# Kernel optimization log

Measured on AMD Instinct MI355X. Metric: run time of the kernel, lower is better.

Reference implementation:

```python
import jax, jax.numpy as jnp
import numpy as np

N_NODES = 100000
N_EDGES = 3200000
N_GRAPHS = 64
IN_DIM = 4
HID = 64
EPS = 1e-5  # BatchNorm eps


def _batchnorm(x, gamma, beta):
    # training-mode batch norm over the node/graph axis (biased variance)
    mu = x.mean(axis=0)
    var = x.var(axis=0)
    return (x - mu) * jax.lax.rsqrt(var + EPS) * gamma + beta


def _gcn_conv(x, W, b, src, dst, n):
    # PyG GCNConv with add_self_loops=True, edge_weight=1:
    # out = D^{-1/2}(A+I)D^{-1/2} x W + b
    h = x @ W  # [N, out]
    deg = jax.ops.segment_sum(jnp.ones((src.shape[0],), h.dtype), dst,
                              num_segments=n) + 1.0  # +1 for self-loop
    dinv = jax.lax.rsqrt(deg)
    norm = dinv[src] * dinv[dst]  # [E]
    agg = jax.ops.segment_sum(h[src] * norm[:, None], dst, num_segments=n)
    # self-loop contribution: norm = 1/deg[i]
    return agg + h * (1.0 / deg)[:, None] + b


def setup_inputs() -> dict:
    key = jax.random.key(0)
    ks = jax.random.split(key, 12)
    s = 0.1
    inp = {
        "x": jax.random.normal(ks[0], (N_NODES, IN_DIM), jnp.float32),
        "edge_index": jax.random.randint(ks[1], (2, N_EDGES), 0, N_NODES, dtype=jnp.int64),
        "batch": jnp.sort(jax.random.randint(ks[2], (N_NODES,), 0, N_GRAPHS, dtype=jnp.int64)),
        # BatchNorm(4)
        "bn0_g": jnp.ones((IN_DIM,), jnp.float32),
        "bn0_b": jnp.zeros((IN_DIM,), jnp.float32),
        # GCNConv(4, 64)
        "W0": jax.random.normal(ks[3], (IN_DIM, HID), jnp.float32) * s,
        "b0": jnp.zeros((HID,), jnp.float32),
        # GCNConv(64, 64)
        "W1": jax.random.normal(ks[4], (HID, HID), jnp.float32) * s,
        "b1": jnp.zeros((HID,), jnp.float32),
        # BatchNorm(64) after pooling
        "bn1_g": jnp.ones((HID,), jnp.float32),
        "bn1_b": jnp.zeros((HID,), jnp.float32),
        # two hidden Linear(64, 64)
        "lin0_W": jax.random.normal(ks[5], (HID, HID), jnp.float32) * s,
        "lin0_b": jnp.zeros((HID,), jnp.float32),
        "lin1_W": jax.random.normal(ks[6], (HID, HID), jnp.float32) * s,
        "lin1_b": jnp.zeros((HID,), jnp.float32),
        # Linear(64, 1)
        "out_W": jax.random.normal(ks[7], (HID, 1), jnp.float32) * s,
        "out_b": jnp.zeros((1,), jnp.float32),
    }
    return inp


def reference(x, edge_index, batch, bn0_g, bn0_b, W0, b0, W1, b1,
              bn1_g, bn1_b, lin0_W, lin0_b, lin1_W, lin1_b, out_W, out_b):
    src, dst = edge_index[0], edge_index[1]
    h = _batchnorm(x, bn0_g, bn0_b)
    h = _gcn_conv(h, W0, b0, src, dst, N_NODES)
    h = _gcn_conv(h, W1, b1, src, dst, N_NODES)
    g = jax.ops.segment_sum(h, batch, num_segments=N_GRAPHS)  # global_add_pool
    g = _batchnorm(g, bn1_g, bn1_b)
    g = g @ lin0_W + lin0_b
    g = g @ lin1_W + lin1_b
    return g @ out_W + out_b  # [N_GRAPHS, 1]
```

## Files before the change

kernel.cpp:

```cpp
#include <hip/hip_runtime.h>
#include <hip/hip_bf16.h>

#define EPSF 1e-5f

static constexpr int NGRAPH = 64;
static constexpr int HBA = 512;
static constexpr int SH = 9;
static constexpr int GB = 256;
static constexpr int CAP = 128;
static constexpr int CAPN = 88;
static constexpr int NBLK = 512;
static constexpr int BNB = 64;
static constexpr int NEL = NGRAPH * 6 + NGRAPH * 4;
static constexpr int RCH = 4;

__global__ __launch_bounds__(256) void k_scat(const float4* __restrict__ x,
                                              int N, const int* __restrict__ ei,
                                              int E, int chunk,
                                              float* __restrict__ bnpart,
                                              unsigned* __restrict__ counts,
                                              unsigned* __restrict__ bedges) {
  __shared__ unsigned cur[256];
  __shared__ float red[4][8];
  int t = threadIdx.x;
  if (blockIdx.x < GB) {
    int g = blockIdx.x;
    cur[t] = 0;
    __syncthreads();
    int lo = g * chunk, hi = min(E, lo + chunk);
    size_t segbase = (size_t)g * 256 * CAP;
    for (int base = lo + 8 * t; base < hi; base += 8 * 256) {
      int nv = min(8, hi - base);
      int s[8], d[8];
#pragma unroll
      for (int j = 0; j < 8; j++) {
        s[j] = (j < nv) ? ei[base + j] : 0;
        d[j] = (j < nv) ? ei[E + base + j] : 0;
      }
      unsigned pos[8], bb[8];
#pragma unroll
      for (int j = 0; j < 8; j++)
        if (j < nv) {
          bb[j] = (unsigned)d[j] >> SH;
          pos[j] = atomicAdd(&cur[bb[j]], 1u);
        }
#pragma unroll
      for (int j = 0; j < 8; j++)
        if (j < nv && pos[j] < (unsigned)CAP)
          bedges[segbase + (size_t)bb[j] * CAP + pos[j]] =
              ((unsigned)s[j] << SH) | (unsigned)(d[j] & (HBA - 1));
    }
    __syncthreads();
    counts[(size_t)g * 256 + t] = min(cur[t], (unsigned)CAP);
  } else {
    int g2 = blockIdx.x - GB;
    float s[4] = {0, 0, 0, 0}, q[4] = {0, 0, 0, 0};
    for (int i = g2 * 256 + t; i < N; i += BNB * 256) {
      float4 v = x[i];
      s[0] += v.x; q[0] += v.x * v.x;
      s[1] += v.y; q[1] += v.y * v.y;
      s[2] += v.z; q[2] += v.z * v.z;
      s[3] += v.w; q[3] += v.w * v.w;
    }
#pragma unroll
    for (int o = 32; o > 0; o >>= 1) {
#pragma unroll
      for (int k = 0; k < 4; k++) {
        s[k] += __shfl_down(s[k], o);
        q[k] += __shfl_down(q[k], o);
      }
    }
    int w = t >> 6;
    if ((t & 63) == 0) {
#pragma unroll
      for (int k = 0; k < 4; k++) {
        red[w][k] = s[k];
        red[w][4 + k] = q[k];
      }
    }
    __syncthreads();
    if (t < 8) {
      float a = red[0][t] + red[1][t] + red[2][t] + red[3][t];
      bnpart[g2 * 8 + t] = a;
    }
  }
}

__device__ __forceinline__ void bn0_coefs(const float* __restrict__ stats,
                                          const float* __restrict__ g,
                                          const float* __restrict__ b,
                                          float Ninv, float* sc, float* sh) {
#pragma unroll
  for (int k = 0; k < 4; k++) {
    float mu = stats[k] * Ninv;
    float var = stats[4 + k] * Ninv - mu * mu;
    var = var < 0.f ? 0.f : var;
    float s = g[k] / sqrtf(var + EPSF);
    sc[k] = s;
    sh[k] = b[k] - mu * s;
  }
}

__global__ __launch_bounds__(512) void k_build(
    const unsigned* __restrict__ bedges, const unsigned* __restrict__ counts,
    const float4* __restrict__ x, int N, const float* __restrict__ bnpart,
    const float* __restrict__ bn0g, const float* __restrict__ bn0b,
    float Ninv, uint4* __restrict__ pk, unsigned* __restrict__ csr) {
  __shared__ unsigned cur[HBA];
  __shared__ unsigned scnt[256];
  __shared__ float sstats[8];
  int t = threadIdx.x;
  int r = blockIdx.x;
  cur[t] = 0;
  if (t < 256) scnt[t] = counts[(size_t)t * 256 + r];
  else if (t < 264) {
    int e = t - 256;
    float s = 0.f;
#pragma unroll 8
    for (int i = 0; i < BNB; i++) s += bnpart[i * 8 + e];
    sstats[e] = s;
  }
  __syncthreads();
  int wv = t >> 6, ln = t & 63;
  size_t nodeBase = (size_t)((unsigned)r << SH) * CAPN;
  for (int g = wv; g < 256; g += 8) {
    unsigned cnt = scnt[g];
    const unsigned* seg = bedges + ((size_t)g * 256 + r) * CAP;
    for (unsigned i = ln; i < cnt; i += 64) {
      unsigned p = seg[i];
      unsigned rel = p & (HBA - 1);
      unsigned pos = atomicAdd(&cur[rel], 1u);
      if (pos < (unsigned)CAPN)
        csr[nodeBase + (size_t)rel * CAPN + pos] = p >> SH;
    }
  }
  __syncthreads();
  unsigned deg = min(cur[t], (unsigned)CAPN);
  int v = (r << SH) + t;
  if (v < N) {
    float sco[4], sho[4];
    bn0_coefs(sstats, bn0g, bn0b, Ninv, sco, sho);
    float dv = rsqrtf((float)deg + 1.0f);
    float4 xv = x[v];
    float zx = dv * (xv.x * sco[0] + sho[0]);
    float zy = dv * (xv.y * sco[1] + sho[1]);
    float zz = dv * (xv.z * sco[2] + sho[2]);
    float zw = dv * (xv.w * sco[3] + sho[3]);
    uint4 u;
    u.x = (__float_as_uint(zx) & ~15u) | (deg & 15u);
    u.y = (__float_as_uint(zy) & ~15u) | ((deg >> 4) & 15u);
    u.z = (__float_as_uint(zz) & ~15u) | ((deg >> 8) & 15u);
    u.w = (__float_as_uint(zw) & ~15u) | ((deg >> 12) & 15u);
    pk[v] = u;
  }
}

__global__ __launch_bounds__(256) void k_acc1f(
    const unsigned* __restrict__ csr, const uint4* __restrict__ pk,
    const int* __restrict__ batch, int N, uint4* __restrict__ p2,
    float* __restrict__ part1) {
  __shared__ float lac[NGRAPH * 6];
  for (int i = threadIdx.x; i < NGRAPH * 6; i += blockDim.x) lac[i] = 0.f;
  __syncthreads();
  int total = gridDim.x * blockDim.x;
  int iters = (N + total - 1) / total;
  int v = blockIdx.x * blockDim.x + threadIdx.x;
  for (int it = 0; it < iters; ++it, v += total) {
    bool act = v < N;
    float u0 = 0, u1 = 0, u2 = 0, u3 = 0, sv = 0, cv = 0;
    int g = 0;
    if (act) {
      uint4 qv = pk[v];
      unsigned deg = (qv.x & 15u) | ((qv.y & 15u) << 4) |
                     ((qv.z & 15u) << 8) | ((qv.w & 15u) << 12);
      unsigned degP = (deg + 3u) & ~3u;
      const uint4* cp = (const uint4*)(csr + (size_t)v * CAPN);
      float a0 = 0, a1 = 0, a2 = 0, a3 = 0, asd = 0;
      for (unsigned e = 0; e < degP; e += 8) {
        uint4 i0 = cp[e >> 2];
        uint4 i1 = cp[(e >> 2) + 1];
        unsigned s[8] = {i0.x, i0.y, i0.z, i0.w, i1.x, i1.y, i1.z, i1.w};
        int m = (int)(deg - e);
        uint4 q[8];
#pragma unroll
        for (int j = 0; j < 8; j++)
          if (j < m) q[j] = pk[s[j]];
#pragma unroll
        for (int j = 0; j < 8; j++)
          if (j < m) {
            unsigned dg = (q[j].x & 15u) | ((q[j].y & 15u) << 4) |
                          ((q[j].z & 15u) << 8) | ((q[j].w & 15u) << 12);
            asd += rsqrtf((float)dg + 1.0f);
            a0 += __uint_as_float(q[j].x);
            a1 += __uint_as_float(q[j].y);
            a2 += __uint_as_float(q[j].z);
            a3 += __uint_as_float(q[j].w);
          }
      }
      float dv = rsqrtf((float)deg + 1.0f);
      float idg = dv * dv;
      float px = idg * (a0 + __uint_as_float(qv.x));
      float py = idg * (a1 + __uint_as_float(qv.y));
      float pz = idg * (a2 + __uint_as_float(qv.z));
      float pw = idg * (a3 + __uint_as_float(qv.w));
      uint4 o;
      o.x = (__float_as_uint(px) & ~15u) | (deg & 15u);
      o.y = (__float_as_uint(py) & ~15u) | ((deg >> 4) & 15u);
      o.z = (__float_as_uint(pz) & ~15u) | ((deg >> 8) & 15u);
      o.w = (__float_as_uint(pw) & ~15u) | ((deg >> 12) & 15u);
      p2[v] = o;
      g = batch[v];
      u0 = dv * __uint_as_float(o.x);
      u1 = dv * __uint_as_float(o.y);
      u2 = dv * __uint_as_float(o.z);
      u3 = dv * __uint_as_float(o.w);
      sv = idg + dv * asd;
      cv = 1.0f;
    }
    if (__all(!act)) continue;
    int gf = __shfl(g, 0);
    bool uni = __all((!act) || (g == gf));
    if (uni) {
#pragma unroll
      for (int o = 32; o > 0; o >>= 1) {
        u0 += __shfl_down(u0, o);
        u1 += __shfl_down(u1, o);
        u2 += __shfl_down(u2, o);
        u3 += __shfl_down(u3, o);
        sv += __shfl_down(sv, o);
        cv += __shfl_down(cv, o);
      }
      if ((threadIdx.x & 63) == 0) {
        int g6 = gf * 6;
        atomicAdd(&lac[g6 + 0], u0);
        atomicAdd(&lac[g6 + 1], u1);
        atomicAdd(&lac[g6 + 2], u2);
        atomicAdd(&lac[g6 + 3], u3);
        atomicAdd(&lac[g6 + 4], sv);
        atomicAdd(&lac[g6 + 5], cv);
      }
    } else if (act) {
      int g6 = g * 6;
      atomicAdd(&lac[g6 + 0], u0);
      atomicAdd(&lac[g6 + 1], u1);
      atomicAdd(&lac[g6 + 2], u2);
      atomicAdd(&lac[g6 + 3], u3);
      atomicAdd(&lac[g6 + 4], sv);
      atomicAdd(&lac[g6 + 5], cv);
    }
  }
  __syncthreads();
  float* out = part1 + (size_t)blockIdx.x * (NGRAPH * 6);
  for (int i = threadIdx.x; i < NGRAPH * 6; i += blockDim.x) out[i] = lac[i];
}

__global__ __launch_bounds__(256) void k_acc2f(
    const unsigned* __restrict__ csr, const uint4* __restrict__ p2,
    const int* __restrict__ batch, int N, float* __restrict__ part2) {
  __shared__ float lac[NGRAPH * 4];
  for (int i = threadIdx.x; i < NGRAPH * 4; i += blockDim.x) lac[i] = 0.f;
  __syncthreads();
  int total = gridDim.x * blockDim.x;
  int iters = (N + total - 1) / total;
  int v = blockIdx.x * blockDim.x + threadIdx.x;
  for (int it = 0; it < iters; ++it, v += total) {
    bool act = v < N;
    float u0 = 0, u1 = 0, u2 = 0, u3 = 0;
    int g = 0;
    if (act) {
      uint4 pv = p2[v];
      unsigned deg = (pv.x & 15u) | ((pv.y & 15u) << 4) |
                     ((pv.z & 15u) << 8) | ((pv.w & 15u) << 12);
      unsigned degP = (deg + 3u) & ~3u;
      const uint4* cp = (const uint4*)(csr + (size_t)v * CAPN);
      float t0 = 0, t1 = 0, t2 = 0, t3 = 0;
      for (unsigned e = 0; e < degP; e += 8) {
        uint4 i0 = cp[e >> 2];
        uint4 i1 = cp[(e >> 2) + 1];
        unsigned s[8] = {i0.x, i0.y, i0.z, i0.w, i1.x, i1.y, i1.z, i1.w};
        int m = (int)(deg - e);
        uint4 q[8];
#pragma unroll
        for (int j = 0; j < 8; j++)
          if (j < m) q[j] = p2[s[j]];
#pragma unroll
        for (int j = 0; j < 8; j++)
          if (j < m) {
            t0 += __uint_as_float(q[j].x);
            t1 += __uint_as_float(q[j].y);
            t2 += __uint_as_float(q[j].z);
            t3 += __uint_as_float(q[j].w);
          }
      }
      float dv = rsqrtf((float)deg + 1.0f);
      g = batch[v];
      u0 = dv * t0; u1 = dv * t1; u2 = dv * t2; u3 = dv * t3;
    }
    if (__all(!act)) continue;
    int gf = __shfl(g, 0);
    bool uni = __all((!act) || (g == gf));
    if (uni) {
#pragma unroll
      for (int o = 32; o > 0; o >>= 1) {
        u0 += __shfl_down(u0, o);
        u1 += __shfl_down(u1, o);
        u2 += __shfl_down(u2, o);
        u3 += __shfl_down(u3, o);
      }
      if ((threadIdx.x & 63) == 0) {
        int g4 = gf * 4;
        atomicAdd(&lac[g4 + 0], u0);
        atomicAdd(&lac[g4 + 1], u1);
        atomicAdd(&lac[g4 + 2], u2);
        atomicAdd(&lac[g4 + 3], u3);
      }
    } else if (act) {
      int g4 = g * 4;
      atomicAdd(&lac[g4 + 0], u0);
      atomicAdd(&lac[g4 + 1], u1);
      atomicAdd(&lac[g4 + 2], u2);
      atomicAdd(&lac[g4 + 3], u3);
    }
  }
  __syncthreads();
  float* out = part2 + (size_t)blockIdx.x * (NGRAPH * 4);
  for (int i = threadIdx.x; i < NGRAPH * 4; i += blockDim.x) out[i] = lac[i];
}

__global__ __launch_bounds__(64) void k_red(const float* __restrict__ part1,
                                            const float* __restrict__ part2,
                                            float* __restrict__ redp) {
  int bid = blockIdx.x;
  int c = bid / 10;
  int eg = bid % 10;
  int e = eg * 64 + threadIdx.x;
  if (e >= NEL) return;
  const float* src;
  int stride, idx;
  if (e < NGRAPH * 6) {
    src = part1; stride = NGRAPH * 6; idx = e;
  } else {
    src = part2; stride = NGRAPH * 4; idx = e - NGRAPH * 6;
  }
  float s = 0.f;
  int b0 = c * (NBLK / RCH);
#pragma unroll 8
  for (int b = 0; b < NBLK / RCH; b++)
    s += src[(size_t)(b0 + b) * stride + idx];
  redp[c * NEL + e] = s;
}

__global__ __launch_bounds__(1024) void k_final(
    const float* __restrict__ redp,
    const float* __restrict__ W0, const float* __restrict__ b0,
    const float* __restrict__ W1, const float* __restrict__ b1,
    const float* __restrict__ bn1g, const float* __restrict__ bn1b,
    const float* __restrict__ l0W, const float* __restrict__ l0b,
    const float* __restrict__ l1W, const float* __restrict__ l1b,
    const float* __restrict__ oW, const float* __restrict__ ob,
    float* __restrict__ out) {
  __shared__ float sP1[NGRAPH * 6];
  __shared__ float sU2[NGRAPH * 4];
  __shared__ float sW01[4 * 64];
  __shared__ float sb01[64];
  __shared__ float sA[4096];
  __shared__ float sB[4096];
  __shared__ float sSc[64], sSh[64];
  __shared__ float wW1[4096], wl0[4096], wl1[4096];
  int t = threadIdx.x;
  for (int i = t; i < 4096; i += 1024) {
    wW1[i] = W1[i];
    wl0[i] = l0W[i];
    wl1[i] = l1W[i];
  }
  if (t < NEL) {
    float s = redp[t] + redp[NEL + t] + redp[2 * NEL + t] + redp[3 * NEL + t];
    if (t < NGRAPH * 6) sP1[t] = s;
    else sU2[t - NGRAPH * 6] = s;
  }
  __syncthreads();
  if (t < 256) {
    int k = t >> 6, f = t & 63;
    float a = 0.f;
#pragma unroll
    for (int j = 0; j < 64; j++) a += W0[k * 64 + j] * wW1[j * 64 + f];
    sW01[t] = a;
  } else if (t < 320) {
    int f = t - 256;
    float a = 0.f;
#pragma unroll
    for (int j = 0; j < 64; j++) a += b0[j] * wW1[j * 64 + f];
    sb01[f] = a;
  }
  __syncthreads();
  for (int idx = t; idx < 4096; idx += 1024) {
    int G = idx >> 6, f = idx & 63;
    float v = sP1[G * 6 + 5] * b1[f] + sP1[G * 6 + 4] * sb01[f];
    v += (sU2[G * 4 + 0] + sP1[G * 6 + 0]) * sW01[0 * 64 + f];
    v += (sU2[G * 4 + 1] + sP1[G * 6 + 1]) * sW01[1 * 64 + f];
    v += (sU2[G * 4 + 2] + sP1[G * 6 + 2]) * sW01[2 * 64 + f];
    v += (sU2[G * 4 + 3] + sP1[G * 6 + 3]) * sW01[3 * 64 + f];
    sA[idx] = v;
  }
  __syncthreads();
  if (t < 64) {
    float mu = 0.f;
#pragma unroll
    for (int G = 0; G < 64; G++) mu += sA[G * 64 + t];
    mu *= (1.0f / 64.0f);
    float var = 0.f;
#pragma unroll
    for (int G = 0; G < 64; G++) {
      float d = sA[G * 64 + t] - mu;
      var += d * d;
    }
    var *= (1.0f / 64.0f);
    float s = bn1g[t] / sqrtf(var + EPSF);
    sSc[t] = s;
    sSh[t] = bn1b[t] - mu * s;
  }
  __syncthreads();
  for (int idx = t; idx < 4096; idx += 1024) {
    int f = idx & 63;
    sA[idx] = sA[idx] * sSc[f] + sSh[f];
  }
  __syncthreads();
  {
    int G = t >> 4, f0 = (t & 15) * 4;
    float a0 = l0b[f0], a1 = l0b[f0 + 1], a2 = l0b[f0 + 2], a3 = l0b[f0 + 3];
#pragma unroll
    for (int j = 0; j < 64; j++) {
      float a = sA[G * 64 + j];
      float4 w = *(const float4*)&wl0[j * 64 + f0];
      a0 += a * w.x; a1 += a * w.y; a2 += a * w.z; a3 += a * w.w;
    }
    *(float4*)&sB[G * 64 + f0] = make_float4(a0, a1, a2, a3);
  }
  __syncthreads();
  {
    int G = t >> 4, f0 = (t & 15) * 4;
    float a0 = l1b[f0], a1 = l1b[f0 + 1], a2 = l1b[f0 + 2], a3 = l1b[f0 + 3];
#pragma unroll
    for (int j = 0; j < 64; j++) {
      float a = sB[G * 64 + j];
      float4 w = *(const float4*)&wl1[j * 64 + f0];
      a0 += a * w.x; a1 += a * w.y; a2 += a * w.z; a3 += a * w.w;
    }
    *(float4*)&sA[G * 64 + f0] = make_float4(a0, a1, a2, a3);
  }
  __syncthreads();
  if (t < 64) {
    float v = ob[0];
#pragma unroll
    for (int j = 0; j < 64; j++) v += sA[t * 64 + j] * oW[j];
    out[t] = v;
  }
}

extern "C" void kernel_launch(void* const* d_in, const int* in_sizes, int n_in,
                              void* d_out, int out_size, void* d_ws,
                              size_t ws_size, hipStream_t stream) {
  const float* x = (const float*)d_in[0];
  const int* ei = (const int*)d_in[1];
  const int* batch = (const int*)d_in[2];
  const float* bn0g = (const float*)d_in[3];
  const float* bn0b = (const float*)d_in[4];
  const float* W0 = (const float*)d_in[5];
  const float* b0 = (const float*)d_in[6];
  const float* W1 = (const float*)d_in[7];
  const float* b1 = (const float*)d_in[8];
  const float* bn1g = (const float*)d_in[9];
  const float* bn1b = (const float*)d_in[10];
  const float* l0W = (const float*)d_in[11];
  const float* l0b = (const float*)d_in[12];
  const float* l1W = (const float*)d_in[13];
  const float* l1b = (const float*)d_in[14];
  const float* oW = (const float*)d_in[15];
  const float* ob = (const float*)d_in[16];

  const int N = in_sizes[0] / 4;
  const int E = in_sizes[1] / 2;
  const int RA = (N + HBA - 1) >> SH;
  const int chunk = (E + GB - 1) / GB;

  size_t off = 0;
  auto alloc = [&](size_t nbytes) {
    size_t cur = (off + 63) & ~(size_t)63;
    off = cur + nbytes;
    return (void*)((char*)d_ws + cur);
  };
  float* bnpart = (float*)alloc((size_t)BNB * 8 * 4);
  float* part1 = (float*)alloc((size_t)NBLK * NGRAPH * 6 * 4);
  float* part2 = (float*)alloc((size_t)NBLK * NGRAPH * 4 * 4);
  float* redp = (float*)alloc((size_t)RCH * NEL * 4);
  uint4* pk = (uint4*)alloc((size_t)N * 16);
  unsigned* counts = (unsigned*)alloc((size_t)GB * 256 * 4);
  unsigned* bedges = (unsigned*)alloc((size_t)GB * 256 * CAP * 4);
  unsigned* csr =
      (unsigned*)alloc(((size_t)RA * HBA * CAPN + 16) * 4);
  uint4* p2 = (uint4*)bedges;
  (void)ws_size;

  const float Ninv = 1.0f / (float)N;
  k_scat<<<GB + BNB, 256, 0, stream>>>((const float4*)x, N, ei, E, chunk,
                                       bnpart, counts, bedges);
  k_build<<<RA, 512, 0, stream>>>(bedges, counts, (const float4*)x, N, bnpart,
                                  bn0g, bn0b, Ninv, pk, csr);
  k_acc1f<<<NBLK, 256, 0, stream>>>(csr, pk, batch, N, p2, part1);
  k_acc2f<<<NBLK, 256, 0, stream>>>(csr, p2, batch, N, part2);
  k_red<<<RCH * 10, 64, 0, stream>>>(part1, part2, redp);
  k_final<<<1, 1024, 0, stream>>>(redp, W0, b0, W1, b1, bn1g, bn1b,
                                  l0W, l0b, l1W, l1b, oW, ob, (float*)d_out);
}
```

Baseline: 224.3 us.

## Split each node's neighbor gather across four lanes and widen scatter blocks

```diff
diff --git a/kernel.cpp b/kernel.cpp
--- a/kernel.cpp
+++ b/kernel.cpp
@@ -9,27 +9,27 @@
 static constexpr int GB = 256;
 static constexpr int CAP = 128;
 static constexpr int CAPN = 88;
-static constexpr int NBLK = 512;
+static constexpr int NBLK = 1568;
 static constexpr int BNB = 64;
 static constexpr int NEL = NGRAPH * 6 + NGRAPH * 4;
-static constexpr int RCH = 4;
-
-__global__ __launch_bounds__(256) void k_scat(const float4* __restrict__ x,
+static constexpr int RCH = 8;
+
+__global__ __launch_bounds__(512) void k_scat(const float4* __restrict__ x,
                                               int N, const int* __restrict__ ei,
                                               int E, int chunk,
                                               float* __restrict__ bnpart,
                                               unsigned* __restrict__ counts,
                                               unsigned* __restrict__ bedges) {
   __shared__ unsigned cur[256];
-  __shared__ float red[4][8];
+  __shared__ float red[8][8];
   int t = threadIdx.x;
   if (blockIdx.x < GB) {
     int g = blockIdx.x;
-    cur[t] = 0;
+    if (t < 256) cur[t] = 0;
     __syncthreads();
     int lo = g * chunk, hi = min(E, lo + chunk);
     size_t segbase = (size_t)g * 256 * CAP;
-    for (int base = lo + 8 * t; base < hi; base += 8 * 256) {
+    for (int base = lo + 8 * t; base < hi; base += 8 * 512) {
       int nv = min(8, hi - base);
       int s[8], d[8];
 #pragma unroll
@@ -51,11 +51,11 @@
               ((unsigned)s[j] << SH) | (unsigned)(d[j] & (HBA - 1));
     }
     __syncthreads();
-    counts[(size_t)g * 256 + t] = min(cur[t], (unsigned)CAP);
+    if (t < 256) counts[(size_t)g * 256 + t] = min(cur[t], (unsigned)CAP);
   } else {
     int g2 = blockIdx.x - GB;
     float s[4] = {0, 0, 0, 0}, q[4] = {0, 0, 0, 0};
-    for (int i = g2 * 256 + t; i < N; i += BNB * 256) {
+    for (int i = g2 * 512 + t; i < N; i += BNB * 512) {
       float4 v = x[i];
       s[0] += v.x; q[0] += v.x * v.x;
       s[1] += v.y; q[1] += v.y * v.y;
@@ -80,7 +80,9 @@
     }
     __syncthreads();
     if (t < 8) {
-      float a = red[0][t] + red[1][t] + red[2][t] + red[3][t];
+      float a = 0.f;
+#pragma unroll
+      for (int w2 = 0; w2 < 8; w2++) a += red[w2][t];
       bnpart[g2 * 8 + t] = a;
     }
   }
@@ -162,62 +164,69 @@
   __shared__ float lac[NGRAPH * 6];
   for (int i = threadIdx.x; i < NGRAPH * 6; i += blockDim.x) lac[i] = 0.f;
   __syncthreads();
-  int total = gridDim.x * blockDim.x;
-  int iters = (N + total - 1) / total;
-  int v = blockIdx.x * blockDim.x + threadIdx.x;
-  for (int it = 0; it < iters; ++it, v += total) {
-    bool act = v < N;
-    float u0 = 0, u1 = 0, u2 = 0, u3 = 0, sv = 0, cv = 0;
-    int g = 0;
-    if (act) {
-      uint4 qv = pk[v];
-      unsigned deg = (qv.x & 15u) | ((qv.y & 15u) << 4) |
-                     ((qv.z & 15u) << 8) | ((qv.w & 15u) << 12);
-      unsigned degP = (deg + 3u) & ~3u;
-      const uint4* cp = (const uint4*)(csr + (size_t)v * CAPN);
-      float a0 = 0, a1 = 0, a2 = 0, a3 = 0, asd = 0;
-      for (unsigned e = 0; e < degP; e += 8) {
-        uint4 i0 = cp[e >> 2];
-        uint4 i1 = cp[(e >> 2) + 1];
-        unsigned s[8] = {i0.x, i0.y, i0.z, i0.w, i1.x, i1.y, i1.z, i1.w};
-        int m = (int)(deg - e);
-        uint4 q[8];
-#pragma unroll
-        for (int j = 0; j < 8; j++)
-          if (j < m) q[j] = pk[s[j]];
-#pragma unroll
-        for (int j = 0; j < 8; j++)
-          if (j < m) {
-            unsigned dg = (q[j].x & 15u) | ((q[j].y & 15u) << 4) |
-                          ((q[j].z & 15u) << 8) | ((q[j].w & 15u) << 12);
-            asd += rsqrtf((float)dg + 1.0f);
-            a0 += __uint_as_float(q[j].x);
-            a1 += __uint_as_float(q[j].y);
-            a2 += __uint_as_float(q[j].z);
-            a3 += __uint_as_float(q[j].w);
-          }
-      }
-      float dv = rsqrtf((float)deg + 1.0f);
-      float idg = dv * dv;
-      float px = idg * (a0 + __uint_as_float(qv.x));
-      float py = idg * (a1 + __uint_as_float(qv.y));
-      float pz = idg * (a2 + __uint_as_float(qv.z));
-      float pw = idg * (a3 + __uint_as_float(qv.w));
-      uint4 o;
-      o.x = (__float_as_uint(px) & ~15u) | (deg & 15u);
-      o.y = (__float_as_uint(py) & ~15u) | ((deg >> 4) & 15u);
-      o.z = (__float_as_uint(pz) & ~15u) | ((deg >> 8) & 15u);
-      o.w = (__float_as_uint(pw) & ~15u) | ((deg >> 12) & 15u);
-      p2[v] = o;
-      g = batch[v];
-      u0 = dv * __uint_as_float(o.x);
-      u1 = dv * __uint_as_float(o.y);
-      u2 = dv * __uint_as_float(o.z);
-      u3 = dv * __uint_as_float(o.w);
-      sv = idg + dv * asd;
-      cv = 1.0f;
-    }
-    if (__all(!act)) continue;
+  int tid = blockIdx.x * blockDim.x + threadIdx.x;
+  int v = tid >> 2, k = tid & 3;
+  bool act = v < N;
+  float a0 = 0, a1 = 0, a2 = 0, a3 = 0, asd = 0;
+  uint4 qv;
+  unsigned deg = 0;
+  if (act) {
+    qv = pk[v];
+    deg = (qv.x & 15u) | ((qv.y & 15u) << 4) | ((qv.z & 15u) << 8) |
+          ((qv.w & 15u) << 12);
+    const uint4* cp = (const uint4*)(csr + (size_t)v * CAPN);
+    for (unsigned e = 4 * k; e < deg; e += 16) {
+      uint4 i0 = cp[e >> 2];
+      unsigned s[4] = {i0.x, i0.y, i0.z, i0.w};
+      int m = (int)(deg - e);
+      uint4 q[4];
+#pragma unroll
+      for (int j = 0; j < 4; j++)
+        if (j < m) q[j] = pk[s[j]];
+#pragma unroll
+      for (int j = 0; j < 4; j++)
+        if (j < m) {
+          unsigned dg = (q[j].x & 15u) | ((q[j].y & 15u) << 4) |
+                        ((q[j].z & 15u) << 8) | ((q[j].w & 15u) << 12);
+          asd += rsqrtf((float)dg + 1.0f);
+          a0 += __uint_as_float(q[j].x);
+          a1 += __uint_as_float(q[j].y);
+          a2 += __uint_as_float(q[j].z);
+          a3 += __uint_as_float(q[j].w);
+        }
+    }
+  }
+#pragma unroll
+  for (int o = 1; o <= 2; o <<= 1) {
+    a0 += __shfl_xor(a0, o);
+    a1 += __shfl_xor(a1, o);
+    a2 += __shfl_xor(a2, o);
+    a3 += __shfl_xor(a3, o);
+    asd += __shfl_xor(asd, o);
+  }
+  float u0 = 0, u1 = 0, u2 = 0, u3 = 0, sv = 0, cv = 0;
+  if (act && k == 0) {
+    float dv = rsqrtf((float)deg + 1.0f);
+    float idg = dv * dv;
+    float px = idg * (a0 + __uint_as_float(qv.x));
+    float py = idg * (a1 + __uint_as_float(qv.y));
+    float pz = idg * (a2 + __uint_as_float(qv.z));
+    float pw = idg * (a3 + __uint_as_float(qv.w));
+    uint4 o;
+    o.x = (__float_as_uint(px) & ~15u) | (deg & 15u);
+    o.y = (__float_as_uint(py) & ~15u) | ((deg >> 4) & 15u);
+    o.z = (__float_as_uint(pz) & ~15u) | ((deg >> 8) & 15u);
+    o.w = (__float_as_uint(pw) & ~15u) | ((deg >> 12) & 15u);
+    p2[v] = o;
+    u0 = dv * __uint_as_float(o.x);
+    u1 = dv * __uint_as_float(o.y);
+    u2 = dv * __uint_as_float(o.z);
+    u3 = dv * __uint_as_float(o.w);
+    sv = idg + dv * asd;
+    cv = 1.0f;
+  }
+  int g = act ? batch[v] : 0;
+  if (!__all(!act)) {
     int gf = __shfl(g, 0);
     bool uni = __all((!act) || (g == gf));
     if (uni) {
@@ -239,7 +248,7 @@
         atomicAdd(&lac[g6 + 4], sv);
         atomicAdd(&lac[g6 + 5], cv);
       }
-    } else if (act) {
+    } else if (act && k == 0) {
       int g6 = g * 6;
       atomicAdd(&lac[g6 + 0], u0);
       atomicAdd(&lac[g6 + 1], u1);
@@ -260,43 +269,48 @@
   __shared__ float lac[NGRAPH * 4];
   for (int i = threadIdx.x; i < NGRAPH * 4; i += blockDim.x) lac[i] = 0.f;
   __syncthreads();
-  int total = gridDim.x * blockDim.x;
-  int iters = (N + total - 1) / total;
-  int v = blockIdx.x * blockDim.x + threadIdx.x;
-  for (int it = 0; it < iters; ++it, v += total) {
-    bool act = v < N;
-    float u0 = 0, u1 = 0, u2 = 0, u3 = 0;
-    int g = 0;
-    if (act) {
-      uint4 pv = p2[v];
-      unsigned deg = (pv.x & 15u) | ((pv.y & 15u) << 4) |
-                     ((pv.z & 15u) << 8) | ((pv.w & 15u) << 12);
-      unsigned degP = (deg + 3u) & ~3u;
-      const uint4* cp = (const uint4*)(csr + (size_t)v * CAPN);
-      float t0 = 0, t1 = 0, t2 = 0, t3 = 0;
-      for (unsigned e = 0; e < degP; e += 8) {
-        uint4 i0 = cp[e >> 2];
-        uint4 i1 = cp[(e >> 2) + 1];
-        unsigned s[8] = {i0.x, i0.y, i0.z, i0.w, i1.x, i1.y, i1.z, i1.w};
-        int m = (int)(deg - e);
-        uint4 q[8];
-#pragma unroll
-        for (int j = 0; j < 8; j++)
-          if (j < m) q[j] = p2[s[j]];
-#pragma unroll
-        for (int j = 0; j < 8; j++)
-          if (j < m) {
-            t0 += __uint_as_float(q[j].x);
-            t1 += __uint_as_float(q[j].y);
-            t2 += __uint_as_float(q[j].z);
-            t3 += __uint_as_float(q[j].w);
-          }
-      }
-      float dv = rsqrtf((float)deg + 1.0f);
-      g = batch[v];
-      u0 = dv * t0; u1 = dv * t1; u2 = dv * t2; u3 = dv * t3;
-    }
-    if (__all(!act)) continue;
+  int tid = blockIdx.x * blockDim.x + threadIdx.x;
+  int v = tid >> 2, k = tid & 3;
+  bool act = v < N;
+  float t0 = 0, t1 = 0, t2 = 0, t3 = 0;
+  unsigned deg = 0;
+  if (act) {
+    uint4 pv = p2[v];
+    deg = (pv.x & 15u) | ((pv.y & 15u) << 4) | ((pv.z & 15u) << 8) |
+          ((pv.w & 15u) << 12);
+    const uint4* cp = (const uint4*)(csr + (size_t)v * CAPN);
+    for (unsigned e = 4 * k; e < deg; e += 16) {
+      uint4 i0 = cp[e >> 2];
+      unsigned s[4] = {i0.x, i0.y, i0.z, i0.w};
+      int m = (int)(deg - e);
+      uint4 q[4];
+#pragma unroll
+      for (int j = 0; j < 4; j++)
+        if (j < m) q[j] = p2[s[j]];
+#pragma unroll
+      for (int j = 0; j < 4; j++)
+        if (j < m) {
+          t0 += __uint_as_float(q[j].x);
+          t1 += __uint_as_float(q[j].y);
+          t2 += __uint_as_float(q[j].z);
+          t3 += __uint_as_float(q[j].w);
+        }
+    }
+  }
+#pragma unroll
+  for (int o = 1; o <= 2; o <<= 1) {
+    t0 += __shfl_xor(t0, o);
+    t1 += __shfl_xor(t1, o);
+    t2 += __shfl_xor(t2, o);
+    t3 += __shfl_xor(t3, o);
+  }
+  float u0 = 0, u1 = 0, u2 = 0, u3 = 0;
+  if (act && k == 0) {
+    float dv = rsqrtf((float)deg + 1.0f);
+    u0 = dv * t0; u1 = dv * t1; u2 = dv * t2; u3 = dv * t3;
+  }
+  int g = act ? batch[v] : 0;
+  if (!__all(!act)) {
     int gf = __shfl(g, 0);
     bool uni = __all((!act) || (g == gf));
     if (uni) {
@@ -314,7 +328,7 @@
         atomicAdd(&lac[g4 + 2], u2);
         atomicAdd(&lac[g4 + 3], u3);
       }
-    } else if (act) {
+    } else if (act && k == 0) {
       int g4 = g * 4;
       atomicAdd(&lac[g4 + 0], u0);
       atomicAdd(&lac[g4 + 1], u1);
@@ -374,7 +388,9 @@
     wl1[i] = l1W[i];
   }
   if (t < NEL) {
-    float s = redp[t] + redp[NEL + t] + redp[2 * NEL + t] + redp[3 * NEL + t];
+    float s = 0.f;
+#pragma unroll
+    for (int c = 0; c < RCH; c++) s += redp[c * NEL + t];
     if (t < NGRAPH * 6) sP1[t] = s;
     else sU2[t - NGRAPH * 6] = s;
   }
@@ -502,7 +518,7 @@
   (void)ws_size;
 
   const float Ninv = 1.0f / (float)N;
-  k_scat<<<GB + BNB, 256, 0, stream>>>((const float4*)x, N, ei, E, chunk,
+  k_scat<<<GB + BNB, 512, 0, stream>>>((const float4*)x, N, ei, E, chunk,
                                        bnpart, counts, bedges);
   k_build<<<RA, 512, 0, stream>>>(bedges, counts, (const float4*)x, N, bnpart,
                                   bn0g, bn0b, Ninv, pk, csr);
```

Result: slower. 229.9 us (+2.5%).
